# Kernel optimization log

Hardware: AMD Instinct MI355X
Metric: run time of the kernel (lower is better)

## Reference

```python
import jax, jax.numpy as jnp
import numpy as np

N_EMBD = 768
N_HEAD = 12
HEAD_DIM = N_EMBD // N_HEAD


def setup_inputs() -> dict:
    key = jax.random.key(0)
    k1, k2, k3, k4, k5 = jax.random.split(key, 5)
    B, T, C = 8, 1024, N_EMBD
    s = 0.02
    return {
        "x": jax.random.normal(k1, (B, T, C), dtype=jnp.float32),
        "w_attn": jax.random.normal(k2, (C, 3 * C), dtype=jnp.float32) * s,
        "b_attn": jnp.zeros((3 * C,), dtype=jnp.float32),
        "w_proj": jax.random.normal(k3, (C, C), dtype=jnp.float32) * s,
        "b_proj": jnp.zeros((C,), dtype=jnp.float32),
    }


def reference(x, w_attn, b_attn, w_proj, b_proj):
    B, T, C = x.shape
    H, D = N_HEAD, HEAD_DIM
    qkv = x @ w_attn + b_attn                      # [B,T,3C]
    q, k, v = jnp.split(qkv, 3, axis=-1)
    # [B,H,T,D]
    q = q.reshape(B, T, H, D).transpose(0, 2, 1, 3)
    k = k.reshape(B, T, H, D).transpose(0, 2, 1, 3)
    v = v.reshape(B, T, H, D).transpose(0, 2, 1, 3)
    att = jnp.einsum("bhqd,bhkd->bhqk", q, k) / jnp.sqrt(jnp.float32(D))
    causal = jnp.tril(jnp.ones((T, T), dtype=bool))
    att = jnp.where(causal[None, None], att, jnp.float32(-jnp.inf))
    att = jax.nn.softmax(att, axis=-1)
    y = jnp.einsum("bhqk,bhkd->bhqd", att, v)      # [B,H,T,D]
    y = y.transpose(0, 2, 1, 3).reshape(B, T, C)
    return y @ w_proj + b_proj
```

## Files before the change

### kernel.cpp

```cpp
#include <hip/hip_runtime.h>
#include <hip/hip_bf16.h>
#include <math.h>
#include <type_traits>

#define BATCH 8
#define SEQ   1024
#define NEMBD 768
#define NHEAD 12
#define HDIM  64
#define TC    (3 * NEMBD)

typedef __attribute__((ext_vector_type(4))) float f32x4;
typedef __attribute__((ext_vector_type(8))) short s16x8;

__device__ __forceinline__ unsigned short f2bf(float f) {
    return __builtin_bit_cast(unsigned short, __float2bfloat16(f));
}

__device__ __forceinline__ void gload_lds16(const void* g, void* l) {
    __builtin_amdgcn_global_load_lds(
        (const __attribute__((address_space(1))) void*)g,
        (__attribute__((address_space(3))) void*)l, 16, 0, 0);
}

__global__ __launch_bounds__(256) void cast_bf16_kernel(
    const float* __restrict__ in, unsigned short* __restrict__ out, int n)
{
    const int i = (blockIdx.x * 256 + threadIdx.x) * 8;
    float4 a = *(const float4*)(in + i);
    float4 b = *(const float4*)(in + i + 4);
    s16x8 v;
    v[0] = f2bf(a.x); v[1] = f2bf(a.y); v[2] = f2bf(a.z); v[3] = f2bf(a.w);
    v[4] = f2bf(b.x); v[5] = f2bf(b.y); v[6] = f2bf(b.z); v[7] = f2bf(b.w);
    *(s16x8*)(out + i) = v;
}

__global__ __launch_bounds__(256) void transpose_cast_kernel(
    const float* __restrict__ w, unsigned short* __restrict__ wT, int K, int N)
{
    __shared__ float t[32][33];
    const int tx = threadIdx.x, ty = threadIdx.y;
    const int n0 = blockIdx.x * 32, k0 = blockIdx.y * 32;
    #pragma unroll
    for (int i = 0; i < 4; ++i)
        t[ty + i * 8][tx] = w[(size_t)(k0 + ty + i * 8) * N + n0 + tx];
    __syncthreads();
    #pragma unroll
    for (int i = 0; i < 4; ++i)
        wT[(size_t)(n0 + ty + i * 8) * K + k0 + tx] = f2bf(t[tx][ty + i * 8]);
}

template <int OUTK>
__global__ __launch_bounds__(256) void gemm_pipe3_kernel(
    const unsigned short* __restrict__ A,
    const unsigned short* __restrict__ Bt,
    const float* __restrict__ bias,
    float* __restrict__ C,
    unsigned short* __restrict__ Qb,
    unsigned short* __restrict__ Kb,
    unsigned short* __restrict__ Vtb,
    int M, int N, int K, int nbn)
{
    constexpr int BUF = 16384;
    __shared__ __align__(16) char SM[3 * BUF];

    const int tid  = threadIdx.x;
    const int w    = tid >> 6, lane = tid & 63;
    const int lr   = lane & 15, lg = lane >> 4;
    const int wr   = w >> 1, wc = w & 1;

    const int swz = (blockIdx.x & 7) * (gridDim.x >> 3) + (blockIdx.x >> 3);
    const int bm = (swz / nbn) * 128, bn = (swz % nbn) * 128;

    const int srow = tid >> 2;
    const int gcol = ((tid & 3) ^ ((srow >> 1) & 3)) * 8;
    const unsigned short* Ag = A  + (size_t)(bm + srow) * K + gcol;
    const unsigned short* Bg = Bt + (size_t)(bn + srow) * K + gcol;

    const int NT = K >> 5;

    f32x4 acc[4][4];
    #pragma unroll
    for (int m = 0; m < 4; ++m)
        #pragma unroll
        for (int n = 0; n < 4; ++n) acc[m][n] = (f32x4){0.f, 0.f, 0.f, 0.f};

    auto stage = [&](int t) {
        const int k0 = t << 5;
        char* buf = SM + (t % 3) * BUF;
        #pragma unroll
        for (int p = 0; p < 2; ++p)
            gload_lds16(Ag + (size_t)(p * 64) * K + k0,
                        buf + p * 4096 + tid * 16);
        #pragma unroll
        for (int p = 0; p < 2; ++p)
            gload_lds16(Bg + (size_t)(p * 64) * K + k0,
                        buf + 8192 + p * 4096 + tid * 16);
    };

    stage(0);
    stage(1);
    asm volatile("s_waitcnt vmcnt(4)" ::: "memory");
    __builtin_amdgcn_sched_barrier(0);
    __builtin_amdgcn_s_barrier();
    __builtin_amdgcn_sched_barrier(0);

    for (int t = 0; t < NT; ++t) {
        const char* buf = SM + (t % 3) * BUF;
        const bool more = (t + 2 < NT);
        if (more) stage(t + 2);

        s16x8 af[4], bfr[4];
        #pragma unroll
        for (int m = 0; m < 4; ++m) {
            const int ar = wr * 64 + m * 16 + lr;
            af[m] = *(const s16x8*)(buf + ar * 64 + ((lg ^ ((ar >> 1) & 3)) * 16));
        }
        #pragma unroll
        for (int n = 0; n < 4; ++n) {
            const int br = wc * 64 + n * 16 + lr;
            bfr[n] = *(const s16x8*)(buf + 8192 + br * 64
                                         + ((lg ^ ((br >> 1) & 3)) * 16));
        }

        __builtin_amdgcn_s_setprio(1);
        #pragma unroll
        for (int m = 0; m < 4; ++m)
            #pragma unroll
            for (int n = 0; n < 4; ++n)
                acc[m][n] = __builtin_amdgcn_mfma_f32_16x16x32_bf16(
                    af[m], bfr[n], acc[m][n], 0, 0, 0);
        __builtin_amdgcn_s_setprio(0);

        if (more) asm volatile("s_waitcnt vmcnt(4)" ::: "memory");
        else      asm volatile("s_waitcnt vmcnt(0)" ::: "memory");
        __builtin_amdgcn_sched_barrier(0);
        __builtin_amdgcn_s_barrier();
        __builtin_amdgcn_sched_barrier(0);
    }

    if constexpr (OUTK == 0) {
        #pragma unroll
        for (int n = 0; n < 4; ++n) {
            const int col = bn + wc * 64 + n * 16 + lr;
            const float bv = bias[col];
            #pragma unroll
            for (int m = 0; m < 4; ++m) {
                const int row0 = bm + wr * 64 + m * 16 + lg * 4;
                #pragma unroll
                for (int r = 0; r < 4; ++r)
                    C[(size_t)(row0 + r) * N + col] = acc[m][n][r] + bv;
            }
        }
    } else {
        char* Ep = SM + w * 8192;

        const int region = bn / NEMBD;
        const int hh = ((bn % NEMBD) >> 6) + wc;
        const int row0 = bm + wr * 64;
        const int bb = row0 >> 10, t0 = row0 & 1023;

        float bvn[4];
        #pragma unroll
        for (int n = 0; n < 4; ++n) bvn[n] = bias[bn + wc * 64 + n * 16 + lr];

        if (region == 2) {
            #pragma unroll
            for (int m = 0; m < 4; ++m)
                #pragma unroll
                for (int n = 0; n < 4; ++n) {
                    ushort4 pk;
                    pk.x = f2bf(acc[m][n][0] + bvn[n]);
                    pk.y = f2bf(acc[m][n][1] + bvn[n]);
                    pk.z = f2bf(acc[m][n][2] + bvn[n]);
                    pk.w = f2bf(acc[m][n][3] + bvn[n]);
                    const int row = n * 16 + lr;
                    const int lc  = m * 2 + (lg >> 1);
                    *(ushort4*)(Ep + row * 128 + ((lc ^ (lr & 7)) * 16)
                                   + (lg & 1) * 8) = pk;
                }
        } else {
            #pragma unroll
            for (int m = 0; m < 4; ++m)
                #pragma unroll
                for (int n = 0; n < 4; ++n)
                    #pragma unroll
                    for (int r = 0; r < 4; ++r) {
                        const int row = m * 16 + lg * 4 + r;
                        const int lc  = n * 2 + (lr >> 3);
                        *(unsigned short*)(Ep + row * 128
                            + ((lc ^ (row & 7)) * 16) + (lr & 7) * 2) =
                            f2bf(acc[m][n][r] + bvn[n]);
                    }
        }
        asm volatile("s_waitcnt lgkmcnt(0)" ::: "memory");
        __builtin_amdgcn_sched_barrier(0);

        const int rr0 = lane >> 3;
        const int cc  = lane & 7;
        if (region == 2) {
            unsigned short* dst = Vtb + (((size_t)bb * NHEAD + hh) * HDIM) * SEQ + t0;
            #pragma unroll
            for (int it = 0; it < 8; ++it) {
                const int d = it * 8 + rr0;
                s16x8 v = *(const s16x8*)(Ep + d * 128 + ((cc ^ (d & 7)) * 16));
                *(s16x8*)(dst + (size_t)d * SEQ + cc * 8) = v;
            }
        } else {
            unsigned short* dst = (region == 0 ? Qb : Kb)
                                + ((size_t)bb * NHEAD + hh) * SEQ * HDIM;
            #pragma unroll
            for (int it = 0; it < 8; ++it) {
                const int t = it * 8 + rr0;
                s16x8 v = *(const s16x8*)(Ep + t * 128 + ((cc ^ (t & 7)) * 16));
                *(s16x8*)(dst + (size_t)(t0 + t) * HDIM + cc * 8) = v;
            }
        }
    }
}

__global__ __launch_bounds__(256) void attn_mfma_kernel(
    const unsigned short* __restrict__ Qb,
    const unsigned short* __restrict__ Kb,
    const unsigned short* __restrict__ Vtb,
    unsigned short* __restrict__ y)
{
    const int bid = blockIdx.x;
    const int xcd = bid & 7;
    const int grp = bid >> 3;
    const int qt  = 15 - (grp & 15);
    const int bh  = xcd + 8 * (grp >> 4);
    const int b   = bh / NHEAD, h = bh % NHEAD;

    const int tid  = threadIdx.x;
    const int w    = tid >> 6;
    const int lane = tid & 63;
    const int lr   = lane & 15;
    const int lg   = lane >> 4;

    __shared__ __align__(16) unsigned short Ks[64 * 64];
    __shared__ __align__(16) unsigned short Vs[64 * 64];
    __shared__ __align__(16) unsigned short Ps[4][16][72];

    const unsigned short* Qg = Qb  + ((size_t)bh * SEQ + qt * 64 + w * 16) * HDIM;
    const unsigned short* Kg = Kb  + (size_t)bh * SEQ * HDIM;
    const unsigned short* Vg = Vtb + (size_t)bh * HDIM * SEQ;

    s16x8 qf[2];
    #pragma unroll
    for (int kc = 0; kc < 2; ++kc)
        qf[kc] = *(const s16x8*)(Qg + (size_t)lr * HDIM + kc * 32 + lg * 8);

    f32x4 acc[4];
    #pragma unroll
    for (int df = 0; df < 4; ++df) acc[df] = (f32x4){0.f, 0.f, 0.f, 0.f};
    float mrow = -INFINITY, lrow = 0.f;

    const int sr = tid >> 2;
    const int sc = (tid & 3) * 16;
    const unsigned short* Kgr = Kg + (size_t)sr * HDIM + sc;
    const unsigned short* Vgr = Vg + (size_t)sr * SEQ  + sc;
    const int swz0 = sr * 128 + ((sc * 2)      ^ ((sr & 7) << 4));
    const int swz1 = sr * 128 + ((sc * 2 + 16) ^ ((sr & 7) << 4));
    const int xorv = (lr & 7) << 4;

    const int NT   = qt + 1;
    const int qrow = qt * 64 + w * 16 + lr;

    s16x8 krA = *(const s16x8*)(Kgr);
    s16x8 krB = *(const s16x8*)(Kgr + 8);
    s16x8 vrA = *(const s16x8*)(Vgr);
    s16x8 vrB = *(const s16x8*)(Vgr + 8);

    for (int kt = 0; kt < NT; ++kt) {
        __syncthreads();
        *(s16x8*)((char*)Ks + swz0) = krA;
        *(s16x8*)((char*)Ks + swz1) = krB;
        *(s16x8*)((char*)Vs + swz0) = vrA;
        *(s16x8*)((char*)Vs + swz1) = vrB;
        __syncthreads();
        if (kt + 1 < NT) {
            krA = *(const s16x8*)(Kgr + (size_t)(kt + 1) * 64 * HDIM);
            krB = *(const s16x8*)(Kgr + (size_t)(kt + 1) * 64 * HDIM + 8);
            vrA = *(const s16x8*)(Vgr + (kt + 1) * 64);
            vrB = *(const s16x8*)(Vgr + (kt + 1) * 64 + 8);
        }

        f32x4 sf[4];
        __builtin_amdgcn_s_setprio(1);
        #pragma unroll
        for (int s = 0; s < 4; ++s) {
            const int rb = (s * 16 + lr) * 128;
            s16x8 a0 = *(const s16x8*)((const char*)Ks + rb + ((lg * 16) ^ xorv));
            s16x8 a1 = *(const s16x8*)((const char*)Ks + rb + ((64 + lg * 16) ^ xorv));
            sf[s] = __builtin_amdgcn_mfma_f32_16x16x32_bf16(
                a0, qf[0], (f32x4){0.f, 0.f, 0.f, 0.f}, 0, 0, 0);
            sf[s] = __builtin_amdgcn_mfma_f32_16x16x32_bf16(a1, qf[1], sf[s], 0, 0, 0);
        }
        __builtin_amdgcn_s_setprio(0);

        float sv[4][4];
        #pragma unroll
        for (int s = 0; s < 4; ++s)
            #pragma unroll
            for (int r = 0; r < 4; ++r)
                sv[s][r] = sf[s][r] * 0.125f;
        if (kt == NT - 1) {
            const int kbase = kt * 64;
            #pragma unroll
            for (int s = 0; s < 4; ++s)
                #pragma unroll
                for (int r = 0; r < 4; ++r)
                    if (kbase + s * 16 + lg * 4 + r > qrow)
                        sv[s][r] = -INFINITY;
        }

        float mx4[4];
        #pragma unroll
        for (int s = 0; s < 4; ++s)
            mx4[s] = fmaxf(fmaxf(sv[s][0], sv[s][1]), fmaxf(sv[s][2], sv[s][3]));
        float mx = fmaxf(fmaxf(mx4[0], mx4[1]), fmaxf(mx4[2], mx4[3]));
        mx = fmaxf(mx, __shfl_xor(mx, 16, 64));
        mx = fmaxf(mx, __shfl_xor(mx, 32, 64));
        const float mnew = fmaxf(mrow, mx);
        const float al   = __expf(mrow - mnew);
        mrow = mnew;

        float rsum = 0.f;
        #pragma unroll
        for (int s = 0; s < 4; ++s) {
            float p0 = __expf(sv[s][0] - mnew);
            float p1 = __expf(sv[s][1] - mnew);
            float p2 = __expf(sv[s][2] - mnew);
            float p3 = __expf(sv[s][3] - mnew);
            rsum += (p0 + p1) + (p2 + p3);
            ushort4 pk;
            pk.x = f2bf(p0); pk.y = f2bf(p1); pk.z = f2bf(p2); pk.w = f2bf(p3);
            *(ushort4*)&Ps[w][lr][s * 16 + lg * 4] = pk;
        }
        rsum += __shfl_xor(rsum, 16, 64);
        rsum += __shfl_xor(rsum, 32, 64);
        lrow = lrow * al + rsum;

        #pragma unroll
        for (int df = 0; df < 4; ++df) acc[df] *= al;

        asm volatile("s_waitcnt lgkmcnt(0)" ::: "memory");
        __builtin_amdgcn_sched_barrier(0);
        s16x8 pa[2];
        #pragma unroll
        for (int kc = 0; kc < 2; ++kc)
            pa[kc] = *(const s16x8*)&Ps[w][lr][kc * 32 + lg * 8];

        __builtin_amdgcn_s_setprio(1);
        #pragma unroll
        for (int df = 0; df < 4; ++df) {
            const int rb = (df * 16 + lr) * 128;
            s16x8 va0 = *(const s16x8*)((const char*)Vs + rb + ((lg * 16) ^ xorv));
            s16x8 va1 = *(const s16x8*)((const char*)Vs + rb + ((64 + lg * 16) ^ xorv));
            acc[df] = __builtin_amdgcn_mfma_f32_16x16x32_bf16(va0, pa[0], acc[df], 0, 0, 0);
            acc[df] = __builtin_amdgcn_mfma_f32_16x16x32_bf16(va1, pa[1], acc[df], 0, 0, 0);
        }
        __builtin_amdgcn_s_setprio(0);
    }

    const float inv = 1.f / lrow;
    const int t = qt * 64 + w * 16 + lr;
    unsigned short* yp = y + ((size_t)(b * SEQ) + t) * NEMBD + h * HDIM;
    #pragma unroll
    for (int df = 0; df < 4; ++df) {
        ushort4 pk;
        pk.x = f2bf(acc[df][0] * inv);
        pk.y = f2bf(acc[df][1] * inv);
        pk.z = f2bf(acc[df][2] * inv);
        pk.w = f2bf(acc[df][3] * inv);
        *(ushort4*)(yp + df * 16 + lg * 4) = pk;
    }
}

extern "C" void kernel_launch(void* const* d_in, const int* in_sizes, int n_in,
                              void* d_out, int out_size, void* d_ws, size_t ws_size,
                              hipStream_t stream)
{
    const float* x      = (const float*)d_in[0];
    const float* w_attn = (const float*)d_in[1];
    const float* b_attn = (const float*)d_in[2];
    const float* w_proj = (const float*)d_in[3];
    const float* b_proj = (const float*)d_in[4];
    float* out = (float*)d_out;

    const int M = BATCH * SEQ;
    const size_t NQKV = (size_t)M * NEMBD;

    unsigned short* xb  = (unsigned short*)d_ws;
    unsigned short* waT = xb  + NQKV;
    unsigned short* wpT = waT + (size_t)TC * NEMBD;
    unsigned short* Qb  = wpT + (size_t)NEMBD * NEMBD;
    unsigned short* Kb  = Qb  + NQKV;
    unsigned short* Vtb = Kb  + NQKV;
    unsigned short* yb  = Vtb + NQKV;

    cast_bf16_kernel<<<(M * NEMBD) / 2048, 256, 0, stream>>>(x, xb, M * NEMBD);
    transpose_cast_kernel<<<dim3(TC / 32, NEMBD / 32), dim3(32, 8), 0, stream>>>(
        w_attn, waT, NEMBD, TC);
    transpose_cast_kernel<<<dim3(NEMBD / 32, NEMBD / 32), dim3(32, 8), 0, stream>>>(
        w_proj, wpT, NEMBD, NEMBD);

    gemm_pipe3_kernel<1><<<(TC / 128) * (M / 128), 256, 0, stream>>>(
        xb, waT, b_attn, nullptr, Qb, Kb, Vtb, M, TC, NEMBD, TC / 128);

    attn_mfma_kernel<<<16 * NHEAD * BATCH, 256, 0, stream>>>(Qb, Kb, Vtb, yb);

    gemm_pipe3_kernel<0><<<(NEMBD / 128) * (M / 128), 256, 0, stream>>>(
        yb, wpT, b_proj, out, nullptr, nullptr, nullptr, M, NEMBD, NEMBD, NEMBD / 128);
}
```

Measured before the change: 116.9 us.

## Pair causal query tiles per block, fold softmax scale into Q, lazy rescale

Each attention block now processes two complementary query tiles (15-p and p), so every block has the same number of key tiles and the causal workload is balanced. The grid shrinks from 1536 to 768 blocks. The 1/sqrt(D)·log2(e) scale is folded into Q in the QKV GEMM epilogue, so the attention loop uses exp2 directly. Rescaling of the running max is skipped unless the max grows by more than 8, which removes per-tile multiplies at some numerical risk. The LDS layout also changes from XOR swizzle to a 72-element padded stride.

```diff
diff --git a/kernel.cpp b/kernel.cpp
--- a/kernel.cpp
+++ b/kernel.cpp
@@ -159,6 +159,7 @@
         const int hh = ((bn % NEMBD) >> 6) + wc;
         const int row0 = bm + wr * 64;
         const int bb = row0 >> 10, t0 = row0 & 1023;
+        const float scl = (region == 0) ? 0.1803368801111354f : 1.0f;
 
         float bvn[4];
         #pragma unroll
@@ -190,7 +191,7 @@
                         const int lc  = n * 2 + (lr >> 3);
                         *(unsigned short*)(Ep + row * 128
                             + ((lc ^ (row & 7)) * 16) + (lr & 7) * 2) =
-                            f2bf(acc[m][n][r] + bvn[n]);
+                            f2bf((acc[m][n][r] + bvn[n]) * scl);
                     }
         }
         asm volatile("s_waitcnt lgkmcnt(0)" ::: "memory");
@@ -225,12 +226,12 @@
     const unsigned short* __restrict__ Vtb,
     unsigned short* __restrict__ y)
 {
-    const int bid = blockIdx.x;
-    const int xcd = bid & 7;
-    const int grp = bid >> 3;
-    const int qt  = 15 - (grp & 15);
-    const int bh  = xcd + 8 * (grp >> 4);
-    const int b   = bh / NHEAD, h = bh % NHEAD;
+    const int bid  = blockIdx.x;
+    const int xcd  = bid & 7;
+    const int grp  = bid >> 3;
+    const int pair = grp & 7;
+    const int bh   = xcd + 8 * (grp >> 3);
+    const int b    = bh / NHEAD, h = bh % NHEAD;
 
     const int tid  = threadIdx.x;
     const int w    = tid >> 6;
@@ -238,144 +239,151 @@
     const int lr   = lane & 15;
     const int lg   = lane >> 4;
 
-    __shared__ __align__(16) unsigned short Ks[64 * 64];
-    __shared__ __align__(16) unsigned short Vs[64 * 64];
+    __shared__ __align__(16) unsigned short Ks[64 * 72];
+    __shared__ __align__(16) unsigned short Vs[64 * 72];
     __shared__ __align__(16) unsigned short Ps[4][16][72];
 
-    const unsigned short* Qg = Qb  + ((size_t)bh * SEQ + qt * 64 + w * 16) * HDIM;
     const unsigned short* Kg = Kb  + (size_t)bh * SEQ * HDIM;
     const unsigned short* Vg = Vtb + (size_t)bh * HDIM * SEQ;
-
-    s16x8 qf[2];
-    #pragma unroll
-    for (int kc = 0; kc < 2; ++kc)
-        qf[kc] = *(const s16x8*)(Qg + (size_t)lr * HDIM + kc * 32 + lg * 8);
-
-    f32x4 acc[4];
-    #pragma unroll
-    for (int df = 0; df < 4; ++df) acc[df] = (f32x4){0.f, 0.f, 0.f, 0.f};
-    float mrow = -INFINITY, lrow = 0.f;
 
     const int sr = tid >> 2;
     const int sc = (tid & 3) * 16;
     const unsigned short* Kgr = Kg + (size_t)sr * HDIM + sc;
     const unsigned short* Vgr = Vg + (size_t)sr * SEQ  + sc;
-    const int swz0 = sr * 128 + ((sc * 2)      ^ ((sr & 7) << 4));
-    const int swz1 = sr * 128 + ((sc * 2 + 16) ^ ((sr & 7) << 4));
-    const int xorv = (lr & 7) << 4;
-
-    const int NT   = qt + 1;
-    const int qrow = qt * 64 + w * 16 + lr;
-
-    s16x8 krA = *(const s16x8*)(Kgr);
-    s16x8 krB = *(const s16x8*)(Kgr + 8);
-    s16x8 vrA = *(const s16x8*)(Vgr);
-    s16x8 vrB = *(const s16x8*)(Vgr + 8);
-
-    for (int kt = 0; kt < NT; ++kt) {
-        __syncthreads();
-        *(s16x8*)((char*)Ks + swz0) = krA;
-        *(s16x8*)((char*)Ks + swz1) = krB;
-        *(s16x8*)((char*)Vs + swz0) = vrA;
-        *(s16x8*)((char*)Vs + swz1) = vrB;
-        __syncthreads();
-        if (kt + 1 < NT) {
-            krA = *(const s16x8*)(Kgr + (size_t)(kt + 1) * 64 * HDIM);
-            krB = *(const s16x8*)(Kgr + (size_t)(kt + 1) * 64 * HDIM + 8);
-            vrA = *(const s16x8*)(Vgr + (kt + 1) * 64);
-            vrB = *(const s16x8*)(Vgr + (kt + 1) * 64 + 8);
-        }
-
-        f32x4 sf[4];
-        __builtin_amdgcn_s_setprio(1);
-        #pragma unroll
-        for (int s = 0; s < 4; ++s) {
-            const int rb = (s * 16 + lr) * 128;
-            s16x8 a0 = *(const s16x8*)((const char*)Ks + rb + ((lg * 16) ^ xorv));
-            s16x8 a1 = *(const s16x8*)((const char*)Ks + rb + ((64 + lg * 16) ^ xorv));
-            sf[s] = __builtin_amdgcn_mfma_f32_16x16x32_bf16(
-                a0, qf[0], (f32x4){0.f, 0.f, 0.f, 0.f}, 0, 0, 0);
-            sf[s] = __builtin_amdgcn_mfma_f32_16x16x32_bf16(a1, qf[1], sf[s], 0, 0, 0);
-        }
-        __builtin_amdgcn_s_setprio(0);
-
-        float sv[4][4];
-        #pragma unroll
-        for (int s = 0; s < 4; ++s)
-            #pragma unroll
-            for (int r = 0; r < 4; ++r)
-                sv[s][r] = sf[s][r] * 0.125f;
-        if (kt == NT - 1) {
-            const int kbase = kt * 64;
+    unsigned short* KsW = Ks + sr * 72 + sc;
+    unsigned short* VsW = Vs + sr * 72 + sc;
+
+    auto process = [&](int qt) {
+        const unsigned short* Qg =
+            Qb + ((size_t)bh * SEQ + qt * 64 + w * 16) * HDIM;
+        s16x8 qf[2];
+        #pragma unroll
+        for (int kc = 0; kc < 2; ++kc)
+            qf[kc] = *(const s16x8*)(Qg + (size_t)lr * HDIM + kc * 32 + lg * 8);
+
+        f32x4 acc[4];
+        #pragma unroll
+        for (int df = 0; df < 4; ++df) acc[df] = (f32x4){0.f, 0.f, 0.f, 0.f};
+        float mrow = -INFINITY, lrow = 0.f;
+
+        const int NT   = qt + 1;
+        const int qrow = qt * 64 + w * 16 + lr;
+
+        s16x8 krA = *(const s16x8*)(Kgr);
+        s16x8 krB = *(const s16x8*)(Kgr + 8);
+        s16x8 vrA = *(const s16x8*)(Vgr);
+        s16x8 vrB = *(const s16x8*)(Vgr + 8);
+
+        for (int kt = 0; kt < NT; ++kt) {
+            __syncthreads();
+            *(s16x8*)(KsW)     = krA;
+            *(s16x8*)(KsW + 8) = krB;
+            *(s16x8*)(VsW)     = vrA;
+            *(s16x8*)(VsW + 8) = vrB;
+            __syncthreads();
+            if (kt + 1 < NT) {
+                krA = *(const s16x8*)(Kgr + (size_t)(kt + 1) * 64 * HDIM);
+                krB = *(const s16x8*)(Kgr + (size_t)(kt + 1) * 64 * HDIM + 8);
+                vrA = *(const s16x8*)(Vgr + (kt + 1) * 64);
+                vrB = *(const s16x8*)(Vgr + (kt + 1) * 64 + 8);
+            }
+
+            f32x4 sf[4];
+            __builtin_amdgcn_s_setprio(1);
+            #pragma unroll
+            for (int s = 0; s < 4; ++s) {
+                const unsigned short* kr = &Ks[(s * 16 + lr) * 72 + lg * 8];
+                s16x8 a0 = *(const s16x8*)(kr);
+                s16x8 a1 = *(const s16x8*)(kr + 32);
+                sf[s] = __builtin_amdgcn_mfma_f32_16x16x32_bf16(
+                    a0, qf[0], (f32x4){0.f, 0.f, 0.f, 0.f}, 0, 0, 0);
+                sf[s] = __builtin_amdgcn_mfma_f32_16x16x32_bf16(a1, qf[1], sf[s], 0, 0, 0);
+            }
+            __builtin_amdgcn_s_setprio(0);
+
+            float sv[4][4];
             #pragma unroll
             for (int s = 0; s < 4; ++s)
                 #pragma unroll
                 for (int r = 0; r < 4; ++r)
-                    if (kbase + s * 16 + lg * 4 + r > qrow)
-                        sv[s][r] = -INFINITY;
-        }
-
-        float mx4[4];
-        #pragma unroll
-        for (int s = 0; s < 4; ++s)
-            mx4[s] = fmaxf(fmaxf(sv[s][0], sv[s][1]), fmaxf(sv[s][2], sv[s][3]));
-        float mx = fmaxf(fmaxf(mx4[0], mx4[1]), fmaxf(mx4[2], mx4[3]));
-        mx = fmaxf(mx, __shfl_xor(mx, 16, 64));
-        mx = fmaxf(mx, __shfl_xor(mx, 32, 64));
-        const float mnew = fmaxf(mrow, mx);
-        const float al   = __expf(mrow - mnew);
-        mrow = mnew;
-
-        float rsum = 0.f;
-        #pragma unroll
-        for (int s = 0; s < 4; ++s) {
-            float p0 = __expf(sv[s][0] - mnew);
-            float p1 = __expf(sv[s][1] - mnew);
-            float p2 = __expf(sv[s][2] - mnew);
-            float p3 = __expf(sv[s][3] - mnew);
-            rsum += (p0 + p1) + (p2 + p3);
+                    sv[s][r] = sf[s][r];
+            if (kt == NT - 1) {
+                const int kbase = kt * 64;
+                #pragma unroll
+                for (int s = 0; s < 4; ++s)
+                    #pragma unroll
+                    for (int r = 0; r < 4; ++r)
+                        if (kbase + s * 16 + lg * 4 + r > qrow)
+                            sv[s][r] = -INFINITY;
+            }
+
+            float mx4[4];
+            #pragma unroll
+            for (int s = 0; s < 4; ++s)
+                mx4[s] = fmaxf(fmaxf(sv[s][0], sv[s][1]), fmaxf(sv[s][2], sv[s][3]));
+            float mx = fmaxf(fmaxf(mx4[0], mx4[1]), fmaxf(mx4[2], mx4[3]));
+            mx = fmaxf(mx, __shfl_xor(mx, 16, 64));
+            mx = fmaxf(mx, __shfl_xor(mx, 32, 64));
+            if (!__all(mx - mrow <= 8.f)) {
+                const float mnew = fmaxf(mrow, mx);
+                const float al   = exp2f(mrow - mnew);
+                lrow *= al;
+                #pragma unroll
+                for (int df = 0; df < 4; ++df) acc[df] *= al;
+                mrow = mnew;
+            }
+
+            float rsum = 0.f;
+            #pragma unroll
+            for (int s = 0; s < 4; ++s) {
+                float p0 = exp2f(sv[s][0] - mrow);
+                float p1 = exp2f(sv[s][1] - mrow);
+                float p2 = exp2f(sv[s][2] - mrow);
+                float p3 = exp2f(sv[s][3] - mrow);
+                rsum += (p0 + p1) + (p2 + p3);
+                ushort4 pk;
+                pk.x = f2bf(p0); pk.y = f2bf(p1); pk.z = f2bf(p2); pk.w = f2bf(p3);
+                *(ushort4*)&Ps[w][lr][s * 16 + lg * 4] = pk;
+            }
+            rsum += __shfl_xor(rsum, 16, 64);
+            rsum += __shfl_xor(rsum, 32, 64);
+            lrow += rsum;
+
+            asm volatile("s_waitcnt lgkmcnt(0)" ::: "memory");
+            __builtin_amdgcn_sched_barrier(0);
+            s16x8 pa[2];
+            #pragma unroll
+            for (int kc = 0; kc < 2; ++kc)
+                pa[kc] = *(const s16x8*)&Ps[w][lr][kc * 32 + lg * 8];
+
+            __builtin_amdgcn_s_setprio(1);
+            #pragma unroll
+            for (int df = 0; df < 4; ++df) {
+                const unsigned short* vr = &Vs[(df * 16 + lr) * 72 + lg * 8];
+                s16x8 va0 = *(const s16x8*)(vr);
+                s16x8 va1 = *(const s16x8*)(vr + 32);
+                acc[df] = __builtin_amdgcn_mfma_f32_16x16x32_bf16(va0, pa[0], acc[df], 0, 0, 0);
+                acc[df] = __builtin_amdgcn_mfma_f32_16x16x32_bf16(va1, pa[1], acc[df], 0, 0, 0);
+            }
+            __builtin_amdgcn_s_setprio(0);
+        }
+
+        const float inv = 1.f / lrow;
+        const int t = qt * 64 + w * 16 + lr;
+        unsigned short* yp = y + ((size_t)(b * SEQ) + t) * NEMBD + h * HDIM;
+        #pragma unroll
+        for (int df = 0; df < 4; ++df) {
             ushort4 pk;
-            pk.x = f2bf(p0); pk.y = f2bf(p1); pk.z = f2bf(p2); pk.w = f2bf(p3);
-            *(ushort4*)&Ps[w][lr][s * 16 + lg * 4] = pk;
-        }
-        rsum += __shfl_xor(rsum, 16, 64);
-        rsum += __shfl_xor(rsum, 32, 64);
-        lrow = lrow * al + rsum;
-
-        #pragma unroll
-        for (int df = 0; df < 4; ++df) acc[df] *= al;
-
-        asm volatile("s_waitcnt lgkmcnt(0)" ::: "memory");
-        __builtin_amdgcn_sched_barrier(0);
-        s16x8 pa[2];
-        #pragma unroll
-        for (int kc = 0; kc < 2; ++kc)
-            pa[kc] = *(const s16x8*)&Ps[w][lr][kc * 32 + lg * 8];
-
-        __builtin_amdgcn_s_setprio(1);
-        #pragma unroll
-        for (int df = 0; df < 4; ++df) {
-            const int rb = (df * 16 + lr) * 128;
-            s16x8 va0 = *(const s16x8*)((const char*)Vs + rb + ((lg * 16) ^ xorv));
-            s16x8 va1 = *(const s16x8*)((const char*)Vs + rb + ((64 + lg * 16) ^ xorv));
-            acc[df] = __builtin_amdgcn_mfma_f32_16x16x32_bf16(va0, pa[0], acc[df], 0, 0, 0);
-            acc[df] = __builtin_amdgcn_mfma_f32_16x16x32_bf16(va1, pa[1], acc[df], 0, 0, 0);
-        }
-        __builtin_amdgcn_s_setprio(0);
-    }
-
-    const float inv = 1.f / lrow;
-    const int t = qt * 64 + w * 16 + lr;
-    unsigned short* yp = y + ((size_t)(b * SEQ) + t) * NEMBD + h * HDIM;
-    #pragma unroll
-    for (int df = 0; df < 4; ++df) {
-        ushort4 pk;
-        pk.x = f2bf(acc[df][0] * inv);
-        pk.y = f2bf(acc[df][1] * inv);
-        pk.z = f2bf(acc[df][2] * inv);
-        pk.w = f2bf(acc[df][3] * inv);
-        *(ushort4*)(yp + df * 16 + lg * 4) = pk;
-    }
+            pk.x = f2bf(acc[df][0] * inv);
+            pk.y = f2bf(acc[df][1] * inv);
+            pk.z = f2bf(acc[df][2] * inv);
+            pk.w = f2bf(acc[df][3] * inv);
+            *(ushort4*)(yp + df * 16 + lg * 4) = pk;
+        }
+    };
+
+    process(15 - pair);
+    process(pair);
 }
 
 extern "C" void kernel_launch(void* const* d_in, const int* in_sizes, int n_in,
@@ -409,7 +417,7 @@
     gemm_pipe3_kernel<1><<<(TC / 128) * (M / 128), 256, 0, stream>>>(
         xb, waT, b_attn, nullptr, Qb, Kb, Vtb, M, TC, NEMBD, TC / 128);
 
-    attn_mfma_kernel<<<16 * NHEAD * BATCH, 256, 0, stream>>>(Qb, Kb, Vtb, yb);
+    attn_mfma_kernel<<<768, 256, 0, stream>>>(Qb, Kb, Vtb, yb);
 
     gemm_pipe3_kernel<0><<<(NEMBD / 128) * (M / 128), 256, 0, stream>>>(
         yb, wpT, b_proj, out, nullptr, nullptr, nullptr, M, NEMBD, NEMBD, NEMBD / 128);
```

Result: faster. 108.9 us (-6.8%).
